# Optimization experiments

Hardware: AMD Instinct MI355X
Metric: run time of the kernel (lower is better)

The kernel has to match this reference:

```python
import jax, jax.numpy as jnp
import numpy as np

NUM_CODES = 1024
EMBED_DIM = 64
COMMITMENT_COST = 0.25
ENTROPY_WEIGHT = 0.1
N_TOKENS = 131072


def setup_inputs() -> dict:
    key = jax.random.key(0)
    k1, k2 = jax.random.split(key)
    z_e = jax.random.normal(k1, (N_TOKENS, EMBED_DIM), dtype=jnp.float32)
    # nn.Embedding init: uniform(-1/num_codes, 1/num_codes)
    codebook = jax.random.uniform(
        k2, (NUM_CODES, EMBED_DIM), dtype=jnp.float32,
        minval=-1.0 / NUM_CODES, maxval=1.0 / NUM_CODES)
    return {"z_e": z_e, "codebook": codebook}


def reference(z_e, codebook):
    # Squared euclidean distances; argmin is invariant to sqrt so skip it.
    # d2[n,k] = |z_n|^2 - 2 z_n.e_k + |e_k|^2
    z_sq = jnp.sum(z_e * z_e, axis=-1, keepdims=True)          # [N,1]
    e_sq = jnp.sum(codebook * codebook, axis=-1)               # [K]
    d2 = z_sq - 2.0 * (z_e @ codebook.T) + e_sq[None, :]       # [N,K]
    indices = jnp.argmin(d2, axis=-1)                          # [N] int

    z_q = codebook[indices]                                    # [N,D] gather

    codebook_loss = jnp.mean((jax.lax.stop_gradient(z_q) - z_e) ** 2)
    commitment_loss = COMMITMENT_COST * jnp.mean(
        (z_q - jax.lax.stop_gradient(z_e)) ** 2)

    # Code-usage histogram via scatter-add (avoids materializing [N,K] one-hot).
    n = z_e.shape[0]
    counts = jnp.zeros((NUM_CODES,), dtype=z_e.dtype).at[indices].add(1.0)
    avg_probs = counts / n + 1e-10
    entropy = -jnp.sum(avg_probs * jnp.log(avg_probs))
    max_entropy = np.log(NUM_CODES)
    entropy_loss = -ENTROPY_WEIGHT * (entropy / max_entropy)
    perplexity = jnp.exp(entropy)

    # Straight-through estimator
    z_q_st = z_e + jax.lax.stop_gradient(z_q - z_e)

    return (z_q_st, indices, codebook_loss, commitment_loss,
            entropy_loss, perplexity)
```

## Files before the change

kernel.cpp:

```cpp
#include <hip/hip_runtime.h>
#include <float.h>
#include <math.h>

#define K_CODES 1024
#define ED 64
#define NTOK 131072
#define EPS 4e-4f

typedef __attribute__((ext_vector_type(8)))  short short8;
typedef __attribute__((ext_vector_type(16))) float float16;


static __device__ __forceinline__ unsigned short f2bf(float x) {
    unsigned u = __float_as_uint(x);
    u += 0x7fffu + ((u >> 16) & 1u);
    return (unsigned short)(u >> 16);
}
static __device__ __forceinline__ float bf2f(unsigned short h) {
    return __uint_as_float(((unsigned)h) << 16);
}

__global__ __launch_bounds__(64) void vq_codes(const float* __restrict__ cb,
                                               float* __restrict__ e_sq,
                                               short8* __restrict__ efH,
                                               short8* __restrict__ efL,
                                               unsigned int* __restrict__ counts,
                                               float* __restrict__ sse_part)
{
#pragma clang fp contract(off)
    const int k = blockIdx.x * 64 + threadIdx.x;
    const float4* ep = (const float4*)(cb + (size_t)k * ED);
    const int m = k & 31, ct = k >> 5;
    float r[8];
#pragma unroll
    for (int g = 0; g < 8; ++g) {
        float4 a = ep[2 * g], b = ep[2 * g + 1];
        float v[8] = {a.x, a.y, a.z, a.w, b.x, b.y, b.z, b.w};
        short8 hv, lv;
#pragma unroll
        for (int j = 0; j < 8; ++j) {
            unsigned short hb = f2bf(v[j]);
            hv[j] = (short)hb;
            lv[j] = (short)f2bf(v[j] - bf2f(hb));
            const float sq = v[j] * v[j];
            r[j] = g ? (r[j] + sq) : sq;
        }
        efH[(ct * 8 + g) * 32 + m] = hv;
        efL[(ct * 8 + g) * 32 + m] = lv;
    }
    e_sq[k] = ((r[0] + r[1]) + (r[2] + r[3])) + ((r[4] + r[5]) + (r[6] + r[7]));
    counts[k]        = 0u;
    counts[k + 1024] = 0u;
    counts[k + 2048] = 0u;
    counts[k + 3072] = 0u;
    if (k < 64) sse_part[k] = 0.f;
}

#define RESCORE(cc)                                                          \
    do {                                                                     \
        const int c_ = (cc);                                                 \
        const float4* e4_ = (const float4*)(cb + (size_t)c_ * ED);           \
        float a_ = 0.f;                                                      \
        _Pragma("unroll")                                                    \
        for (int jj_ = 0; jj_ < 16; ++jj_) {                                 \
            const float4 v_ = e4_[jj_];                                      \
            a_ = fmaf(zr[4 * jj_ + 0], v_.x, a_);                            \
            a_ = fmaf(zr[4 * jj_ + 1], v_.y, a_);                            \
            a_ = fmaf(zr[4 * jj_ + 2], v_.z, a_);                            \
            a_ = fmaf(zr[4 * jj_ + 3], v_.w, a_);                            \
        }                                                                    \
        const float d2_ = fmaf(-2.f, a_, zsq) + e_sq[c_];                    \
        if (d2_ < best || (d2_ == best && c_ < bi)) { best = d2_; bi = c_; } \
    } while (0)

#define SEL_STRIDE 65

__global__ __launch_bounds__(256, 3) void vq_main(const float* __restrict__ z_e,
                                                  const float* __restrict__ cb,
                                                  const float* __restrict__ e_sq,
                                                  const short8* __restrict__ efH,
                                                  const short8* __restrict__ efL,
                                                  float* __restrict__ out_zq,
                                                  float* __restrict__ out_idx,
                                                  unsigned int* __restrict__ counts,
                                                  float* __restrict__ sse_part)
{
#pragma clang fp contract(off)
    __shared__ short8 s_zfh[512];
    __shared__ short8 s_zfl[512];
    __shared__ float2 s_sel[32 * SEL_STRIDE];
    __shared__ int    s_bi[64];
    __shared__ float  s_wsse[4];

    const int tid = threadIdx.x;
    const int wv = tid >> 6, lane = tid & 63;
    const int h = lane >> 5, ml = lane & 31;
    const int t0 = blockIdx.x * 64;

    {
        const float4* zp = (const float4*)(z_e + (size_t)(t0 + lane) * ED);
        const int n = lane & 31, ttl = lane >> 5;
#pragma unroll
        for (int gg = 0; gg < 2; ++gg) {
            const int g = wv * 2 + gg;
            float4 a = zp[2 * g], b = zp[2 * g + 1];
            float v[8] = {a.x, a.y, a.z, a.w, b.x, b.y, b.z, b.w};
            short8 hv, lv;
#pragma unroll
            for (int j = 0; j < 8; ++j) {
                unsigned short hb = f2bf(v[j]);
                hv[j] = (short)hb;
                lv[j] = (short)f2bf(v[j] - bf2f(hb));
            }
            s_zfh[(ttl * 8 + g) * 32 + n] = hv;
            s_zfl[(ttl * 8 + g) * 32 + n] = lv;
        }
    }
    __syncthreads();

#pragma unroll
    for (int g = 0; g < 4; ++g) {
        short8 ea[2][4], eb[2][4];
#pragma unroll
        for (int mt = 0; mt < 2; ++mt) {
            const int ct = g * 8 + wv * 2 + mt;
#pragma unroll
            for (int q = 0; q < 4; ++q) {
                const int idx = (ct * 8 + q * 2 + h) * 32 + ml;
                ea[mt][q] = efH[idx];
                eb[mt][q] = efL[idx];
            }
        }
#pragma unroll
        for (int it = 0; it < 2; ++it) {
            float16 acc0 = {}, acc1 = {};
#pragma unroll
            for (int q = 0; q < 4; ++q) {
                const int idx = (it * 8 + q * 2 + h) * 32 + ml;
                const short8 zh = s_zfh[idx];
                const short8 zl = s_zfl[idx];
                acc0 = __builtin_amdgcn_mfma_f32_32x32x16_bf16(ea[0][q], zh, acc0, 0, 0, 0);
                acc1 = __builtin_amdgcn_mfma_f32_32x32x16_bf16(ea[1][q], zh, acc1, 0, 0, 0);
                acc0 = __builtin_amdgcn_mfma_f32_32x32x16_bf16(ea[0][q], zl, acc0, 0, 0, 0);
                acc1 = __builtin_amdgcn_mfma_f32_32x32x16_bf16(ea[1][q], zl, acc1, 0, 0, 0);
                acc0 = __builtin_amdgcn_mfma_f32_32x32x16_bf16(eb[0][q], zh, acc0, 0, 0, 0);
                acc1 = __builtin_amdgcn_mfma_f32_32x32x16_bf16(eb[1][q], zh, acc1, 0, 0, 0);
            }
#pragma unroll
            for (int mt = 0; mt < 2; ++mt) {
                const float16 acc = mt ? acc1 : acc0;
                float tv1[8], tv2[8];
                int   ti[8];
#pragma unroll
                for (int p = 0; p < 8; ++p) {
                    const float a = acc[2 * p], b = acc[2 * p + 1];
                    const int ia = ((2 * p) & 3) + 8 * ((2 * p) >> 2) + 4 * h;
                    const int ib = ((2 * p + 1) & 3) + 8 * ((2 * p + 1) >> 2) + 4 * h;
                    const bool gt = b > a;
                    tv1[p] = gt ? b : a;
                    ti[p]  = gt ? ib : ia;
                    tv2[p] = gt ? a : b;
                }
#pragma unroll
                for (int s = 4; s >= 1; s >>= 1) {
#pragma unroll
                    for (int p = 0; p < s; ++p) {
                        const float av1 = tv1[2 * p], bv1 = tv1[2 * p + 1];
                        const bool gt = bv1 > av1;
                        const float inner = gt ? av1 : bv1;
                        tv1[p] = gt ? bv1 : av1;
                        ti[p]  = gt ? ti[2 * p + 1] : ti[2 * p];
                        tv2[p] = fmaxf(fmaxf(tv2[2 * p], tv2[2 * p + 1]), inner);
                    }
                }
                float v1 = tv1[0], v2 = tv2[0];
                int i1 = ti[0];
                const float o1 = __shfl_xor(v1, 32);
                const float o2 = __shfl_xor(v2, 32);
                const int   oi = __shfl_xor(i1, 32);
                const float lo = fminf(v1, o1);
                if (o1 > v1) { v1 = o1; i1 = oi; }
                v2 = fmaxf(lo, fmaxf(v2, o2));
                if (lane < 32) {
                    const unsigned bits = (__float_as_uint(-2.f * v1) & ~31u) | (unsigned)i1;
                    float2 o;
                    o.x = __uint_as_float(bits);
                    o.y = -2.f * v2;
                    s_sel[(g * 8 + wv * 2 + mt) * SEL_STRIDE + it * 32 + lane] = o;
                }
            }
        }
    }

    const float4* z4  = (const float4*)z_e + (size_t)t0 * 16;
    float4 zv[4];
#pragma unroll
    for (int p = 0; p < 4; ++p) zv[p] = z4[p * 256 + tid];
    __syncthreads();

    {
        const int tls = tid >> 2;
        const int sub = tid & 3;
        const int t = t0 + tls;

        float av[8], bv[8];
        float m = FLT_MAX;
#pragma unroll
        for (int i = 0; i < 8; ++i) {
            const float2 p = s_sel[(sub * 8 + i) * SEL_STRIDE + tls];
            av[i] = p.x; bv[i] = p.y;
            m = fminf(m, av[i]);
        }
        m = fminf(m, __shfl_xor(m, 1));
        m = fminf(m, __shfl_xor(m, 2));
        const float thr = m + EPS;

        unsigned band8 = 0u, full8 = 0u;
        int cand0 = 0, nb = 0;
#pragma unroll
        for (int i = 0; i < 8; ++i) {
            if (av[i] <= thr) {
                if (nb == 0)
                    cand0 = (sub * 8 + i) * 32 + (int)(__float_as_uint(av[i]) & 31u);
                ++nb;
                band8 |= (1u << i);
                if (bv[i] <= thr) full8 |= (1u << i);
            }
        }
        int fullany = (full8 != 0u);
        {
            int nb_o = __shfl_xor(nb, 1);
            int c0_o = __shfl_xor(cand0, 1);
            int fa_o = __shfl_xor(fullany, 1);
            cand0 = ((sub & 1) == 0) ? (nb ? cand0 : c0_o) : (nb_o ? c0_o : cand0);
            nb += nb_o; fullany |= fa_o;
            nb_o = __shfl_xor(nb, 2);
            c0_o = __shfl_xor(cand0, 2);
            fa_o = __shfl_xor(fullany, 2);
            cand0 = ((sub & 2) == 0) ? (nb ? cand0 : c0_o) : (nb_o ? c0_o : cand0);
            nb += nb_o; fullany |= fa_o;
        }

        int bsel;
        if (nb == 1 && !fullany) {
            bsel = cand0;
        } else {
            const float4* zp = (const float4*)(z_e + (size_t)t * ED);
            float zr[ED];
#pragma unroll
            for (int i = 0; i < 16; ++i) {
                const float4 v = zp[i];
                zr[4 * i + 0] = v.x; zr[4 * i + 1] = v.y;
                zr[4 * i + 2] = v.z; zr[4 * i + 3] = v.w;
            }
            float r[8];
#pragma unroll
            for (int g2 = 0; g2 < 8; ++g2) {
#pragma unroll
                for (int j = 0; j < 8; ++j) {
                    const float sq = zr[g2 * 8 + j] * zr[g2 * 8 + j];
                    r[j] = g2 ? (r[j] + sq) : sq;
                }
            }
            const float zsq = ((r[0] + r[1]) + (r[2] + r[3])) + ((r[4] + r[5]) + (r[6] + r[7]));
            float best = FLT_MAX;
            int bi = 0;
            unsigned rem = band8;
            while (rem) {
                const int i = __ffs(rem) - 1;
                rem &= rem - 1;
                const int ct = sub * 8 + i;
                if (full8 & (1u << i)) {
                    for (int j = 0; j < 32; ++j) RESCORE(ct * 32 + j);
                } else {
                    RESCORE(ct * 32 + (int)(__float_as_uint(av[i]) & 31u));
                }
            }
#pragma unroll
            for (int d = 1; d <= 2; d <<= 1) {
                const float ob  = __shfl_xor(best, d);
                const int   obi = __shfl_xor(bi, d);
                if (ob < best || (ob == best && obi < bi)) { best = ob; bi = obi; }
            }
            bsel = bi;
        }

        if (sub == 0) {
            s_bi[tls] = bsel;
            out_idx[t] = (float)bsel;
            atomicAdd(&counts[(blockIdx.x & 3) * K_CODES + bsel], 1u);
        }
    }
    __syncthreads();

    float4* o4 = (float4*)out_zq + (size_t)t0 * 16;
    const float4* eq4 = (const float4*)cb;
    float lsse = 0.f;
#pragma unroll
    for (int p = 0; p < 4; ++p) {
        const int f = p * 256 + tid;
        const int bq = s_bi[f >> 4];
        const float4 q = eq4[(size_t)bq * 16 + (f & 15)];
        o4[f] = q;
        float dx = q.x - zv[p].x; lsse = fmaf(dx, dx, lsse);
        float dy = q.y - zv[p].y; lsse = fmaf(dy, dy, lsse);
        float dz = q.z - zv[p].z; lsse = fmaf(dz, dz, lsse);
        float dw = q.w - zv[p].w; lsse = fmaf(dw, dw, lsse);
    }
#pragma unroll
    for (int off = 32; off > 0; off >>= 1)
        lsse += __shfl_down(lsse, off, 64);
    if (lane == 0) s_wsse[wv] = lsse;
    __syncthreads();
    if (tid == 0)
        atomicAdd(&sse_part[blockIdx.x & 63],
                  (s_wsse[0] + s_wsse[1]) + (s_wsse[2] + s_wsse[3]));
}

__global__ __launch_bounds__(1024) void vq_final(const unsigned int* __restrict__ counts,
                                                 const float* __restrict__ sse_part,
                                                 float* __restrict__ out_sc)
{
    __shared__ float red[1024];
    const int i = threadIdx.x;
    const unsigned int cu = counts[i] + counts[i + 1024]
                          + counts[i + 2048] + counts[i + 3072];
    const float c = (float)cu;
    const float p = c / (float)NTOK + 1e-10f;
    red[i] = p * logf(p);
    __syncthreads();
    for (int s = 512; s > 0; s >>= 1) {
        if (i < s) red[i] += red[i + s];
        __syncthreads();
    }
    if (i == 0) {
        const float entropy = -red[0];
        float ssum = 0.f;
        for (int k = 0; k < 64; ++k) ssum += sse_part[k];
        const float cbl = ssum / ((float)NTOK * (float)ED);
        out_sc[0] = cbl;
        out_sc[1] = 0.25f * cbl;
        out_sc[2] = -0.1f * (entropy / 6.93147180559945f);
        out_sc[3] = expf(entropy);
    }
}

extern "C" void kernel_launch(void* const* d_in, const int* in_sizes, int n_in,
                              void* d_out, int out_size, void* d_ws, size_t ws_size,
                              hipStream_t stream)
{
    const float* z_e = (const float*)d_in[0];
    const float* cb  = (const float*)d_in[1];

    float* out   = (float*)d_out;
    float* o_zq  = out;
    float* o_idx = out + (size_t)NTOK * ED;
    float* o_sc  = o_idx + NTOK;

    char* ws = (char*)d_ws;
    float*        e_sq     = (float*)(ws);
    unsigned int* counts   = (unsigned int*)(ws + 4096);
    float*        sse_part = (float*)(ws + 20480);
    short8*       efH      = (short8*)(ws + 32768);
    short8*       efL      = (short8*)(ws + 163840);

    vq_codes<<<16, 64, 0, stream>>>(cb, e_sq, efH, efL, counts, sse_part);
    vq_main <<<NTOK / 64, 256, 0, stream>>>(z_e, cb, e_sq, efH, efL,
                                            o_zq, o_idx, counts, sse_part);
    vq_final<<<1, 1024, 0, stream>>>(counts, sse_part, o_sc);
}
```

Before: 167.4 us.

## Parallelize codebook prep, lower main kernel occupancy bound, warp-reduce SSE

The codebook preprocessing kernel now uses 256 threads per block. Each block stages 64 codebook rows in padded shared memory, and four threads split the bf16 hi/lo conversion of each row. This targets the small serial prologue kernel. Separately, the main kernel's launch bounds hint drops from 3 to 2 blocks per SM, giving the compiler more registers at the cost of occupancy. The final kernel replaces its serial 64-element SSE sum with a wave shuffle reduction.

```diff
diff --git a/kernel.cpp b/kernel.cpp
--- a/kernel.cpp
+++ b/kernel.cpp
@@ -20,40 +20,68 @@
     return __uint_as_float(((unsigned)h) << 16);
 }
 
-__global__ __launch_bounds__(64) void vq_codes(const float* __restrict__ cb,
-                                               float* __restrict__ e_sq,
-                                               short8* __restrict__ efH,
-                                               short8* __restrict__ efL,
-                                               unsigned int* __restrict__ counts,
-                                               float* __restrict__ sse_part)
+__global__ __launch_bounds__(256) void vq_codes(const float* __restrict__ cb,
+                                                float* __restrict__ e_sq,
+                                                short8* __restrict__ efH,
+                                                short8* __restrict__ efL,
+                                                unsigned int* __restrict__ counts,
+                                                float* __restrict__ sse_part)
 {
 #pragma clang fp contract(off)
-    const int k = blockIdx.x * 64 + threadIdx.x;
-    const float4* ep = (const float4*)(cb + (size_t)k * ED);
-    const int m = k & 31, ct = k >> 5;
-    float r[8];
-#pragma unroll
-    for (int g = 0; g < 8; ++g) {
-        float4 a = ep[2 * g], b = ep[2 * g + 1];
-        float v[8] = {a.x, a.y, a.z, a.w, b.x, b.y, b.z, b.w};
-        short8 hv, lv;
-#pragma unroll
-        for (int j = 0; j < 8; ++j) {
-            unsigned short hb = f2bf(v[j]);
-            hv[j] = (short)hb;
-            lv[j] = (short)f2bf(v[j] - bf2f(hb));
-            const float sq = v[j] * v[j];
-            r[j] = g ? (r[j] + sq) : sq;
-        }
-        efH[(ct * 8 + g) * 32 + m] = hv;
-        efL[(ct * 8 + g) * 32 + m] = lv;
-    }
-    e_sq[k] = ((r[0] + r[1]) + (r[2] + r[3])) + ((r[4] + r[5]) + (r[6] + r[7]));
-    counts[k]        = 0u;
-    counts[k + 1024] = 0u;
-    counts[k + 2048] = 0u;
-    counts[k + 3072] = 0u;
-    if (k < 64) sse_part[k] = 0.f;
+    __shared__ float s_cb[64 * 68];
+    const int tid = threadIdx.x;
+    const int k0 = blockIdx.x * 64;
+
+    const float4* cb4 = (const float4*)(cb + (size_t)k0 * ED);
+#pragma unroll
+    for (int p = 0; p < 4; ++p) {
+        const int f = p * 256 + tid;
+        const float4 v = cb4[f];
+        float4* dst = (float4*)&s_cb[(f >> 4) * 68 + (f & 15) * 4];
+        *dst = v;
+    }
+    __syncthreads();
+
+    {
+        const int c = tid >> 2, sub = tid & 3;
+        const int k = k0 + c;
+        const int m = k & 31, ct = k >> 5;
+#pragma unroll
+        for (int gg = 0; gg < 2; ++gg) {
+            const int g = sub * 2 + gg;
+            const float4 a = *(const float4*)&s_cb[c * 68 + g * 8];
+            const float4 b = *(const float4*)&s_cb[c * 68 + g * 8 + 4];
+            float v[8] = {a.x, a.y, a.z, a.w, b.x, b.y, b.z, b.w};
+            short8 hv, lv;
+#pragma unroll
+            for (int j = 0; j < 8; ++j) {
+                unsigned short hb = f2bf(v[j]);
+                hv[j] = (short)hb;
+                lv[j] = (short)f2bf(v[j] - bf2f(hb));
+            }
+            efH[(ct * 8 + g) * 32 + m] = hv;
+            efL[(ct * 8 + g) * 32 + m] = lv;
+        }
+    }
+
+    if (tid < 64) {
+        float r[8];
+#pragma unroll
+        for (int g = 0; g < 8; ++g) {
+            const float4 a = *(const float4*)&s_cb[tid * 68 + g * 8];
+            const float4 b = *(const float4*)&s_cb[tid * 68 + g * 8 + 4];
+            float v[8] = {a.x, a.y, a.z, a.w, b.x, b.y, b.z, b.w};
+#pragma unroll
+            for (int j = 0; j < 8; ++j) {
+                const float sq = v[j] * v[j];
+                r[j] = g ? (r[j] + sq) : sq;
+            }
+        }
+        e_sq[k0 + tid] = ((r[0] + r[1]) + (r[2] + r[3])) + ((r[4] + r[5]) + (r[6] + r[7]));
+    }
+
+    counts[blockIdx.x * 256 + tid] = 0u;
+    if (blockIdx.x == 0 && tid < 64) sse_part[tid] = 0.f;
 }
 
 #define RESCORE(cc)                                                          \
@@ -75,7 +103,7 @@
 
 #define SEL_STRIDE 65
 
-__global__ __launch_bounds__(256, 3) void vq_main(const float* __restrict__ z_e,
+__global__ __launch_bounds__(256, 2) void vq_main(const float* __restrict__ z_e,
                                                   const float* __restrict__ cb,
                                                   const float* __restrict__ e_sq,
                                                   const short8* __restrict__ efH,
@@ -322,12 +350,20 @@
                                                  float* __restrict__ out_sc)
 {
     __shared__ float red[1024];
+    __shared__ float s_ssum;
     const int i = threadIdx.x;
     const unsigned int cu = counts[i] + counts[i + 1024]
                           + counts[i + 2048] + counts[i + 3072];
     const float c = (float)cu;
     const float p = c / (float)NTOK + 1e-10f;
     red[i] = p * logf(p);
+    if (i < 64) {
+        float s = sse_part[i];
+#pragma unroll
+        for (int off = 32; off > 0; off >>= 1)
+            s += __shfl_down(s, off, 64);
+        if (i == 0) s_ssum = s;
+    }
     __syncthreads();
     for (int s = 512; s > 0; s >>= 1) {
         if (i < s) red[i] += red[i + s];
@@ -335,9 +371,7 @@
     }
     if (i == 0) {
         const float entropy = -red[0];
-        float ssum = 0.f;
-        for (int k = 0; k < 64; ++k) ssum += sse_part[k];
-        const float cbl = ssum / ((float)NTOK * (float)ED);
+        const float cbl = s_ssum / ((float)NTOK * (float)ED);
         out_sc[0] = cbl;
         out_sc[1] = 0.25f * cbl;
         out_sc[2] = -0.1f * (entropy / 6.93147180559945f);
@@ -364,7 +398,7 @@
     short8*       efH      = (short8*)(ws + 32768);
     short8*       efL      = (short8*)(ws + 163840);
 
-    vq_codes<<<16, 64, 0, stream>>>(cb, e_sq, efH, efL, counts, sse_part);
+    vq_codes<<<16, 256, 0, stream>>>(cb, e_sq, efH, efL, counts, sse_part);
     vq_main <<<NTOK / 64, 256, 0, stream>>>(z_e, cb, e_sq, efH, efL,
                                             o_zq, o_idx, counts, sse_part);
     vq_final<<<1, 1024, 0, stream>>>(counts, sse_part, o_sc);
```

New measurement: 165.7 us. No clear change (-1.0%).
